# Performance work log

Measured on AMD Instinct MI355X. Metric: run time of the kernel, lower is better.

## Reference

```python
import jax, jax.numpy as jnp
import numpy as np

D_IN, D_KQ, D_V = 1024, 1024, 1024
SEQ = 4096


def setup_inputs() -> dict:
    key = jax.random.key(0)
    k1, k2, k3, k4 = jax.random.split(key, 4)
    x = jax.random.normal(k1, (SEQ, D_IN), dtype=jnp.float32)
    # original uses torch.rand (uniform [0,1)) for params
    W_query = jax.random.uniform(k2, (D_IN, D_KQ), dtype=jnp.float32)
    W_key = jax.random.uniform(k3, (D_IN, D_KQ), dtype=jnp.float32)
    W_value = jax.random.uniform(k4, (D_IN, D_V), dtype=jnp.float32)
    return {"x": x, "W_query": W_query, "W_key": W_key, "W_value": W_value}


def reference(x, W_query, W_key, W_value):
    # x: [S, d_in]
    queries = x @ W_query          # [S, d_kq]
    keys = x @ W_key               # [S, d_kq]
    values = x @ W_value           # [S, d_v]
    scale = 1.0 / jnp.sqrt(jnp.asarray(D_KQ, dtype=x.dtype))
    attn_scores = (queries @ keys.T) * scale   # [S, S]
    attn_weights = jax.nn.softmax(attn_scores, axis=-1)
    return attn_weights @ values   # [S, d_v]
```

## Files before the change

### kernel.cpp

```cpp
#include <hip/hip_runtime.h>


typedef _Float16 f16;
typedef f16 f16x8 __attribute__((ext_vector_type(8)));
typedef f16 f16x4v __attribute__((ext_vector_type(4)));
typedef float f32x4 __attribute__((ext_vector_type(4)));
typedef float f32x16 __attribute__((ext_vector_type(16)));
typedef unsigned short u16;
typedef u16 u16x8 __attribute__((ext_vector_type(8)));

extern __shared__ char dsm[];

__device__ __forceinline__ void split_f32(float v, f16& h, f16& l) {
  h = (f16)v;
  l = (f16)(v - (float)h);
}

__device__ __forceinline__ void gload16(const void* g, void* l) {
  __builtin_amdgcn_global_load_lds(
      (const __attribute__((address_space(1))) void*)g,
      (__attribute__((address_space(3))) void*)l, 16, 0, 0);
}

__global__ __launch_bounds__(256) void k_prep(
    const float* __restrict__ x, const float* __restrict__ Wq,
    const float* __restrict__ Wk, const float* __restrict__ Wv,
    f16* __restrict__ xh, f16* __restrict__ xl, f16* __restrict__ wqh,
    f16* __restrict__ wql, f16* __restrict__ wkh, f16* __restrict__ wkl,
    f16* __restrict__ wvt, float* __restrict__ sa, float* __restrict__ sb) {
  const int y = blockIdx.y;
  if (y <= 2) {
    const float* __restrict__ src = (y == 0) ? x : (y == 1) ? Wq : Wk;
    f16* __restrict__ oh = (y == 0) ? xh : (y == 1) ? wqh : wkh;
    f16* __restrict__ ol = (y == 0) ? xl : (y == 1) ? wql : wkl;
    const int n4 = (y == 0) ? (4096 * 1024 / 4) : (1024 * 1024 / 4);
    for (int i = blockIdx.x * 256 + threadIdx.x; i < n4; i += 1024 * 256) {
      float4 f = ((const float4*)src)[i];
      f16x4v h, l;
      f16 hh, ll;
      split_f32(f.x, hh, ll); h[0] = hh; l[0] = ll;
      split_f32(f.y, hh, ll); h[1] = hh; l[1] = ll;
      split_f32(f.z, hh, ll); h[2] = hh; l[2] = ll;
      split_f32(f.w, hh, ll); h[3] = hh; l[3] = ll;
      ((f16x4v*)oh)[i] = h;
      ((f16x4v*)ol)[i] = l;
    }
  } else if (y == 3) {
    if (blockIdx.x >= 256) return;
    __shared__ float sh[64][65];
    const int kb = (blockIdx.x >> 4) * 64, nb = (blockIdx.x & 15) * 64;
    const int t = threadIdx.x;
    const int r = t >> 2, c4 = (t & 3) * 16;
#pragma unroll
    for (int i = 0; i < 4; ++i) {
      float4 f = *(const float4*)&Wv[(size_t)(kb + r) * 1024 + nb + c4 + i * 4];
      sh[r][c4 + i * 4 + 0] = f.x;
      sh[r][c4 + i * 4 + 1] = f.y;
      sh[r][c4 + i * 4 + 2] = f.z;
      sh[r][c4 + i * 4 + 3] = f.w;
    }
    __syncthreads();
    const int n = t >> 2, ks = (t & 3) * 16;
    u16x8 h0, h1;
#pragma unroll
    for (int i = 0; i < 8; ++i) {
      h0[i] = __builtin_bit_cast(u16, (f16)sh[ks + i][n]);
      h1[i] = __builtin_bit_cast(u16, (f16)sh[ks + 8 + i][n]);
    }
    const size_t o = (size_t)(nb + n) * 1024 + kb + ks;
    *(u16x8*)&wvt[o] = h0;
    *(u16x8*)&wvt[o + 8] = h1;
  } else {
    if (blockIdx.x >= 512) return;
    const int z = blockIdx.x >> 8;
    const float* __restrict__ W = z ? Wk : Wq;
    float* __restrict__ o = z ? sb : sa;
    const int row = (blockIdx.x & 255) * 4 + (threadIdx.x >> 6);
    const int lane = threadIdx.x & 63;
    const float4* src = (const float4*)(W + (size_t)row * 1024);
    float s = 0.f;
#pragma unroll
    for (int i = 0; i < 4; ++i) {
      float4 f = src[lane + 64 * i];
      s += f.x + f.y + f.z + f.w;
    }
#pragma unroll
    for (int off = 1; off < 64; off <<= 1) s += __shfl_xor(s, off, 64);
    if (lane == 0) o[row] = s - 512.0f;
  }
}

__global__ __launch_bounds__(256) void k_rpq(
    const float* __restrict__ x, const float* __restrict__ sa,
    const float* __restrict__ sb, float* __restrict__ rv,
    float* __restrict__ pv, float* __restrict__ qv) {
  const int row = blockIdx.x * 4 + (threadIdx.x >> 6);
  const int lane = threadIdx.x & 63;
  const float* xr = x + (size_t)row * 1024;
  float sr = 0.f, sp = 0.f, sq = 0.f;
#pragma unroll
  for (int i = 0; i < 4; ++i) {
    const int c = (lane + 64 * i) * 4;
    float4 f = *(const float4*)&xr[c];
    float4 a = *(const float4*)&sa[c];
    float4 b = *(const float4*)&sb[c];
    sr += f.x + f.y + f.z + f.w;
    sp += f.x * a.x + f.y * a.y + f.z * a.z + f.w * a.w;
    sq += f.x * b.x + f.y * b.y + f.z * b.z + f.w * b.w;
  }
#pragma unroll
  for (int off = 1; off < 64; off <<= 1) {
    sr += __shfl_xor(sr, off, 64);
    sp += __shfl_xor(sp, off, 64);
    sq += __shfl_xor(sq, off, 64);
  }
  if (lane == 0) {
    rv[row] = sr;
    pv[row] = sp;
    qv[row] = sq;
  }
}

__global__ __launch_bounds__(512, 1) void k_qkt(
    const f16* __restrict__ Ah, const f16* __restrict__ Bx,
    const float* __restrict__ rv, const float* __restrict__ pv,
    const float* __restrict__ qv, f16* __restrict__ Pt,
    float* __restrict__ mtile, float* __restrict__ tsum) {
  char* smem = dsm;
  constexpr int K = 1024, N = 4096, nT = 32, BUF = 32768;
  const int tid = threadIdx.x;
  const int lane = tid & 63, wv = tid >> 6;
  const int bid = blockIdx.x;
  const int wg = (bid & 7) * 32 + (bid >> 3);
  const int bx = wg >> 4, by = wg & 15;
  const int brow = bx * 256, bcol = by * 256;

  const int srow16 = lane >> 2;
  const int sslot = (lane & 3) ^ ((lane >> 3) & 3);

  const f16* bases[2] = {Ah, Bx};
  const int rbase[2] = {brow, bcol};

  auto stage2 = [&](int buf, int t, int half) {
    const int kt = t * 32;
    char* bb = smem + BUF * buf;
#pragma unroll
    for (int j = 0; j < 2; ++j) {
      const int g = wv * 4 + half * 2 + j;
      const int rg = g >> 4, gm = g & 15;
      gload16(
          bases[rg] + (size_t)(rbase[rg] + gm * 16 + srow16) * K + kt + 8 * sslot,
          bb + rg * 16384 + gm * 1024);
    }
  };

  f32x16 acc[8] = {};
  const int l31 = lane & 31, ch0 = lane >> 5;
  const int arow = wv * 32 + l31;

  stage2(0, 0, 0);
  stage2(0, 0, 1);

  for (int t = 0; t < nT; ++t) {
    const int cur = t & 1;
    const char* bb = smem + BUF * cur;
    const bool pre = t < nT - 1;
    if (pre) {
      stage2(cur ^ 1, t + 1, 0);
      __builtin_amdgcn_sched_barrier(0);
      asm volatile("s_waitcnt vmcnt(2)" ::: "memory");
    } else {
      asm volatile("s_waitcnt vmcnt(0)" ::: "memory");
    }
    __builtin_amdgcn_sched_barrier(0);
    __builtin_amdgcn_s_barrier();
    __builtin_amdgcn_sched_barrier(0);

    f16x8 a_h0, b_h0[8];
    {
      const int ch = ch0;
      a_h0 = *(const f16x8*)(bb + arow * 64 + 16 * (ch ^ ((arow >> 1) & 3)));
#pragma unroll
      for (int fn = 0; fn < 8; ++fn) {
        const int r = fn * 32 + l31;
        b_h0[fn] = *(const f16x8*)(bb + 16384 + r * 64 +
                                   16 * (ch ^ ((r >> 1) & 3)));
      }
    }
    if (pre) stage2(cur ^ 1, t + 1, 1);
    asm volatile("s_waitcnt lgkmcnt(0)" ::: "memory");
    __builtin_amdgcn_sched_barrier(0);
    __builtin_amdgcn_s_setprio(1);
#pragma unroll
    for (int fn = 0; fn < 8; ++fn)
      acc[fn] = __builtin_amdgcn_mfma_f32_32x32x16_f16(a_h0, b_h0[fn], acc[fn],
                                                       0, 0, 0);
    __builtin_amdgcn_s_setprio(0);

    f16x8 a_h1, b_h1[8];
    {
      const int ch = 2 + ch0;
      a_h1 = *(const f16x8*)(bb + arow * 64 + 16 * (ch ^ ((arow >> 1) & 3)));
#pragma unroll
      for (int fn = 0; fn < 8; ++fn) {
        const int r = fn * 32 + l31;
        b_h1[fn] = *(const f16x8*)(bb + 16384 + r * 64 +
                                   16 * (ch ^ ((r >> 1) & 3)));
      }
    }
    asm volatile("s_waitcnt lgkmcnt(0)" ::: "memory");
    __builtin_amdgcn_sched_barrier(0);
    __builtin_amdgcn_s_setprio(1);
#pragma unroll
    for (int fn = 0; fn < 8; ++fn)
      acc[fn] = __builtin_amdgcn_mfma_f32_32x32x16_f16(a_h1, b_h1[fn], acc[fn],
                                                       0, 0, 0);
    __builtin_amdgcn_s_setprio(0);
    __builtin_amdgcn_sched_barrier(0);
    __builtin_amdgcn_s_barrier();
  }

  float rc[8], qc[8];
#pragma unroll
  for (int fn = 0; fn < 8; ++fn) {
    const int col = bcol + fn * 32 + l31;
    rc[fn] = rv[col];
    qc[fn] = qv[col];
  }
  const int rowbase = brow + wv * 32;
#pragma unroll
  for (int j = 0; j < 16; ++j) {
    const int rl = (j & 3) + 8 * (j >> 2) + 4 * ch0;
    const int row = rowbase + rl;
    const float rr = rv[row], pr = pv[row];
    float s[8];
    float m = -3.4e38f;
#pragma unroll
    for (int fn = 0; fn < 8; ++fn) {
      s[fn] = acc[fn][j] + 8.0f * rr * rc[fn] + (pr * rc[fn] + rr * qc[fn]) * 0.015625f;
      m = fmaxf(m, s[fn]);
    }
#pragma unroll
    for (int off = 1; off < 32; off <<= 1) m = fmaxf(m, __shfl_xor(m, off, 64));
    float sm = 0.f;
#pragma unroll
    for (int fn = 0; fn < 8; ++fn) {
      const float e = __expf(s[fn] - m);
      sm += e;
      Pt[(size_t)row * N + bcol + fn * 32 + l31] = (f16)e;
    }
#pragma unroll
    for (int off = 1; off < 32; off <<= 1) sm += __shfl_xor(sm, off, 64);
    if (l31 == 0) {
      mtile[row * 16 + by] = m;
      tsum[row * 16 + by] = sm;
    }
  }
}

__global__ __launch_bounds__(512, 1) void k_pvs(const f16* __restrict__ P,
                                                const f16* __restrict__ Vt,
                                                const float* __restrict__ mtile,
                                                const float* __restrict__ tsum,
                                                float* __restrict__ out) {
  char* smem = dsm;
  constexpr int K = 4096, nT = K / 32, BUF = 16384;
  const int tid = threadIdx.x;
  const int lane = tid & 63, wv = tid >> 6;
  const int wm = wv >> 2, wn = wv & 3;
  const int bid = blockIdx.x;
  const int wg = (bid & 7) * 32 + (bid >> 3);
  const int bx = wg >> 3, by = wg & 7;
  const int brow = bx * 128, bcol = by * 128;

  const int srow16 = lane >> 2;
  const int sslot = (lane & 3) ^ ((lane >> 3) & 3);
  const int sreg = wv >> 2;
  const f16* __restrict__ sbase = sreg ? Vt : P;
  const int rbase = sreg ? bcol : brow;

  float* sc_lds = (float*)(smem + 4 * BUF);
  if (tid < 128) {
    const int row = brow + tid;
    float mt[16], ts[16];
    float m = -3.4e38f;
#pragma unroll
    for (int t4 = 0; t4 < 4; ++t4) {
      float4 v = *(const float4*)&mtile[row * 16 + t4 * 4];
      float4 w = *(const float4*)&tsum[row * 16 + t4 * 4];
      mt[t4 * 4 + 0] = v.x; mt[t4 * 4 + 1] = v.y;
      mt[t4 * 4 + 2] = v.z; mt[t4 * 4 + 3] = v.w;
      ts[t4 * 4 + 0] = w.x; ts[t4 * 4 + 1] = w.y;
      ts[t4 * 4 + 2] = w.z; ts[t4 * 4 + 3] = w.w;
      m = fmaxf(m, fmaxf(fmaxf(v.x, v.y), fmaxf(v.z, v.w)));
    }
    float sum = 0.f;
#pragma unroll
    for (int t = 0; t < 16; ++t) sum += ts[t] * __expf(mt[t] - m);
    const float inv = 1.0f / sum;
#pragma unroll
    for (int t = 0; t < 16; ++t)
      sc_lds[t * 128 + tid] = __expf(mt[t] - m) * inv;
  }
  __syncthreads();

  auto stage = [&](int buf, int t) {
    const int kt = t * 32;
    char* bb = smem + BUF * buf + sreg * 8192;
#pragma unroll
    for (int j = 0; j < 2; ++j) {
      const int g = (wv & 3) * 2 + j;
      gload16(sbase + (size_t)(rbase + g * 16 + srow16) * K + kt + 8 * sslot,
              bb + g * 1024);
    }
  };

  f32x16 accp[2] = {};
  f32x16 accf[2] = {};
  const int l31 = lane & 31, ch0 = lane >> 5;
  const int arow0 = wm * 64 + l31;
  const int brow0 = wn * 32 + l31;

  stage(0, 0);
  stage(1, 1);
  stage(2, 2);

  for (int t = 0; t < nT; ++t) {
    const int rem = nT - 1 - t;
    if (rem >= 3) stage((t + 3) & 3, t + 3);
    __builtin_amdgcn_sched_barrier(0);
    if (rem >= 3) {
      asm volatile("s_waitcnt vmcnt(6)" ::: "memory");
    } else if (rem == 2) {
      asm volatile("s_waitcnt vmcnt(4)" ::: "memory");
    } else if (rem == 1) {
      asm volatile("s_waitcnt vmcnt(2)" ::: "memory");
    } else {
      asm volatile("s_waitcnt vmcnt(0)" ::: "memory");
    }
    __builtin_amdgcn_sched_barrier(0);
    __builtin_amdgcn_s_barrier();
    __builtin_amdgcn_sched_barrier(0);
    const char* bb = smem + BUF * (t & 3);
#pragma unroll
    for (int ks = 0; ks < 2; ++ks) {
      const int ch = ks * 2 + ch0;
      f16x8 a_h[2], b_h;
#pragma unroll
      for (int fm = 0; fm < 2; ++fm) {
        const int r = arow0 + fm * 32;
        a_h[fm] = *(const f16x8*)(bb + r * 64 + 16 * (ch ^ ((r >> 1) & 3)));
      }
      b_h = *(const f16x8*)(bb + 8192 + brow0 * 64 +
                            16 * (ch ^ ((brow0 >> 1) & 3)));
      __builtin_amdgcn_sched_barrier(0);
      asm volatile("s_waitcnt lgkmcnt(0)" ::: "memory");
      __builtin_amdgcn_sched_barrier(0);
      __builtin_amdgcn_s_setprio(1);
#pragma unroll
      for (int fm = 0; fm < 2; ++fm)
        accp[fm] = __builtin_amdgcn_mfma_f32_32x32x16_f16(a_h[fm], b_h,
                                                          accp[fm], 0, 0, 0);
      __builtin_amdgcn_s_setprio(0);
      __builtin_amdgcn_sched_barrier(0);
    }
    if ((t & 7) == 7) {
      const int tc = t >> 3;
#pragma unroll
      for (int fm = 0; fm < 2; ++fm)
#pragma unroll
        for (int j = 0; j < 16; ++j) {
          const int rloc =
              wm * 64 + fm * 32 + (j & 3) + 8 * (j >> 2) + 4 * ch0;
          accf[fm][j] += sc_lds[tc * 128 + rloc] * accp[fm][j];
          accp[fm][j] = 0.0f;
        }
    }
    __builtin_amdgcn_s_barrier();
  }

#pragma unroll
  for (int fm = 0; fm < 2; ++fm) {
    const int col = bcol + wn * 32 + l31;
#pragma unroll
    for (int j = 0; j < 16; ++j) {
      const int row =
          brow + wm * 64 + fm * 32 + (j & 3) + 8 * (j >> 2) + 4 * ch0;
      out[(size_t)row * 1024 + col] = accf[fm][j];
    }
  }
}

template <int K, int NBY>
__global__ __launch_bounds__(512, 1) void pipe_bt(const f16* __restrict__ A,
                                                  const f16* __restrict__ B,
                                                  f16* __restrict__ outh,
                                                  int ldo) {
  char* smem = dsm;
  constexpr int nT = K / 32, BUF = 16384;
  const int tid = threadIdx.x;
  const int lane = tid & 63, wv = tid >> 6;
  const int wm = wv >> 2, wn = wv & 3;
  const int bid = blockIdx.x;
  const int wg = (bid & 7) * 32 + (bid >> 3);
  const int bx = wg / NBY, by = wg % NBY;
  const int brow = bx * 128, bcol = by * 128;

  const int srow16 = lane >> 2;
  const int sslot = (lane & 3) ^ ((lane >> 3) & 3);
  const int sreg = wv >> 2;
  const f16* __restrict__ sbase = sreg ? B : A;
  const int rbase = sreg ? bcol : brow;

  auto stage = [&](int buf, int t) {
    const int kt = t * 32;
    char* bb = smem + BUF * buf + sreg * 8192;
#pragma unroll
    for (int j = 0; j < 2; ++j) {
      const int g = (wv & 3) * 2 + j;
      gload16(sbase + (size_t)(rbase + g * 16 + srow16) * K + kt + 8 * sslot,
              bb + g * 1024);
    }
  };

  f32x16 acc[2] = {};
  const int l31 = lane & 31, ch0 = lane >> 5;
  const int arow0 = wm * 64 + l31;
  const int brow0 = wn * 32 + l31;

  stage(0, 0);
  stage(1, 1);
  stage(2, 2);

  for (int t = 0; t < nT; ++t) {
    const int rem = nT - 1 - t;
    if (rem >= 3) stage((t + 3) & 3, t + 3);
    __builtin_amdgcn_sched_barrier(0);
    if (rem >= 3) {
      asm volatile("s_waitcnt vmcnt(6)" ::: "memory");
    } else if (rem == 2) {
      asm volatile("s_waitcnt vmcnt(4)" ::: "memory");
    } else if (rem == 1) {
      asm volatile("s_waitcnt vmcnt(2)" ::: "memory");
    } else {
      asm volatile("s_waitcnt vmcnt(0)" ::: "memory");
    }
    __builtin_amdgcn_sched_barrier(0);
    __builtin_amdgcn_s_barrier();
    __builtin_amdgcn_sched_barrier(0);
    const char* bb = smem + BUF * (t & 3);
#pragma unroll
    for (int ks = 0; ks < 2; ++ks) {
      const int ch = ks * 2 + ch0;
      f16x8 a_h[2], b_h;
#pragma unroll
      for (int fm = 0; fm < 2; ++fm) {
        const int r = arow0 + fm * 32;
        a_h[fm] = *(const f16x8*)(bb + r * 64 + 16 * (ch ^ ((r >> 1) & 3)));
      }
      b_h = *(const f16x8*)(bb + 8192 + brow0 * 64 +
                            16 * (ch ^ ((brow0 >> 1) & 3)));
      __builtin_amdgcn_sched_barrier(0);
      asm volatile("s_waitcnt lgkmcnt(0)" ::: "memory");
      __builtin_amdgcn_sched_barrier(0);
      __builtin_amdgcn_s_setprio(1);
#pragma unroll
      for (int fm = 0; fm < 2; ++fm)
        acc[fm] = __builtin_amdgcn_mfma_f32_32x32x16_f16(a_h[fm], b_h, acc[fm],
                                                         0, 0, 0);
      __builtin_amdgcn_s_setprio(0);
      __builtin_amdgcn_sched_barrier(0);
    }
    __builtin_amdgcn_s_barrier();
  }

#pragma unroll
  for (int fm = 0; fm < 2; ++fm) {
    const int col = bcol + wn * 32 + l31;
#pragma unroll
    for (int j = 0; j < 16; ++j) {
      const int row =
          brow + wm * 64 + fm * 32 + (j & 3) + 8 * (j >> 2) + 4 * ch0;
      outh[(size_t)row * ldo + col] = (f16)acc[fm][j];
    }
  }
}

template <int NM, int OUT>
__global__ __launch_bounds__(256) void gemm_bt(
    const f16* __restrict__ A, const f16* __restrict__ Al,
    const f16* __restrict__ B, const f16* __restrict__ Bl, int K,
    f16* __restrict__ oh, f16* __restrict__ ol, int ldo, float scale,
    const float* __restrict__ sav, const float* __restrict__ sbv) {
  f16* smem = (f16*)dsm;
  f16* tAh = smem;
  f16* tBh = smem + 8192;
  f16* tAl = smem + 16384;
  f16* tBl = smem + 24576;

  const int tid = threadIdx.x;
  const int lane = tid & 63, wid = tid >> 6;
  const int wr = wid >> 1, wc = wid & 1;
  const int brow = blockIdx.x * 128, bcol = blockIdx.y * 128;
  const int ar = lane & 15, k0 = (lane >> 4) * 8;
  const int crow = lane >> 3, ccol = (lane & 7) * 8;

  f32x4 acc[4][4] = {};
  const size_t aoff = (size_t)crow * K + ccol;

  for (int kt = 0; kt < K; kt += 64) {
    const f16* Ab = A + (size_t)brow * K + kt;
    const f16* Bb = B + (size_t)bcol * K + kt;
#pragma unroll
    for (int cc = 0; cc < 4; ++cc) {
      const int c = wid * 4 + cc;
      const size_t co = (size_t)c * 8 * K + aoff;
      gload16(Ab + co, tAh + c * 512);
      gload16(Bb + co, tBh + c * 512);
      if constexpr (NM >= 2) gload16(Al + (size_t)brow * K + kt + co, tAl + c * 512);
      if constexpr (NM == 3) gload16(Bl + (size_t)bcol * K + kt + co, tBl + c * 512);
    }
    __syncthreads();
#pragma unroll
    for (int ks = 0; ks < 2; ++ks) {
      f16x8 ah[4], bh[4], alv[4], blv[4];
#pragma unroll
      for (int m = 0; m < 4; ++m) {
        ah[m] = *(const f16x8*)&tAh[(wr * 64 + m * 16 + ar) * 64 + ks * 32 + k0];
        bh[m] = *(const f16x8*)&tBh[(wc * 64 + m * 16 + ar) * 64 + ks * 32 + k0];
        if constexpr (NM >= 2)
          alv[m] = *(const f16x8*)&tAl[(wr * 64 + m * 16 + ar) * 64 + ks * 32 + k0];
        if constexpr (NM == 3)
          blv[m] = *(const f16x8*)&tBl[(wc * 64 + m * 16 + ar) * 64 + ks * 32 + k0];
      }
#pragma unroll
      for (int m = 0; m < 4; ++m)
#pragma unroll
        for (int n = 0; n < 4; ++n) {
          acc[m][n] = __builtin_amdgcn_mfma_f32_16x16x32_f16(ah[m], bh[n], acc[m][n], 0, 0, 0);
          if constexpr (NM >= 2)
            acc[m][n] = __builtin_amdgcn_mfma_f32_16x16x32_f16(alv[m], bh[n], acc[m][n], 0, 0, 0);
          if constexpr (NM == 3)
            acc[m][n] = __builtin_amdgcn_mfma_f32_16x16x32_f16(ah[m], blv[n], acc[m][n], 0, 0, 0);
        }
    }
    __syncthreads();
  }

#pragma unroll
  for (int m = 0; m < 4; ++m)
#pragma unroll
    for (int n = 0; n < 4; ++n)
#pragma unroll
      for (int j = 0; j < 4; ++j) {
        const int row = brow + wr * 64 + m * 16 + (lane >> 4) * 4 + j;
        const int col = bcol + wc * 64 + n * 16 + ar;
        const size_t idx = (size_t)row * ldo + col;
        if constexpr (OUT == 1) {
          f16 h, l;
          split_f32(acc[m][n][j] * scale, h, l);
          oh[idx] = h;
          ol[idx] = l;
        } else if constexpr (OUT == 2) {
          oh[idx] = (f16)(acc[m][n][j] * scale);
        } else {
          const float v =
              (acc[m][n][j] - 256.0f - 0.5f * sav[col] - 0.5f * sbv[row]) * scale;
          oh[idx] = (f16)v;
        }
      }
}

extern "C" void kernel_launch(void* const* d_in, const int* in_sizes, int n_in,
                              void* d_out, int out_size, void* d_ws,
                              size_t ws_size, hipStream_t stream) {
  const float* x = (const float*)d_in[0];
  const float* Wq = (const float*)d_in[1];
  const float* Wk = (const float*)d_in[2];
  const float* Wv = (const float*)d_in[3];
  float* out = (float*)d_out;
  char* ws = (char*)d_ws;
  const size_t MiB = 1u << 20;
  f16* xh = (f16*)(ws + 0 * MiB);
  f16* xl = (f16*)(ws + 8 * MiB);
  f16* Th = (f16*)(ws + 16 * MiB);
  f16* Vt = (f16*)(ws + 32 * MiB);
  f16* Pt = (f16*)(ws + 40 * MiB);
  float* mtile = (float*)(ws + 72 * MiB);
  float* tsum = (float*)(ws + 73 * MiB);
  f16* Wqh = (f16*)(ws + 40 * MiB);
  f16* Wql = (f16*)(ws + 42 * MiB);
  f16* Wkh = (f16*)(ws + 44 * MiB);
  f16* Wkl = (f16*)(ws + 46 * MiB);
  f16* Mth = (f16*)(ws + 48 * MiB);
  f16* Wtvh = (f16*)(ws + 52 * MiB);
  float* sa = (float*)(ws + 54 * MiB);
  float* sb = (float*)(ws + 54 * MiB + 65536);
  float* rv = (float*)(ws + 8 * MiB);
  float* pv = (float*)(ws + 8 * MiB + 65536);
  float* qv = (float*)(ws + 8 * MiB + 131072);

  (void)hipFuncSetAttribute((const void*)k_qkt,
                            hipFuncAttributeMaxDynamicSharedMemorySize, 65536);
  (void)hipFuncSetAttribute((const void*)k_pvs,
                            hipFuncAttributeMaxDynamicSharedMemorySize, 73728);
  (void)hipFuncSetAttribute((const void*)pipe_bt<1024, 32>,
                            hipFuncAttributeMaxDynamicSharedMemorySize, 65536);

  k_prep<<<dim3(1024, 5), 256, 0, stream>>>(x, Wq, Wk, Wv, xh, xl, Wqh, Wql,
                                            Wkh, Wkl, Wtvh, sa, sb);
  gemm_bt<3, 4><<<dim3(8, 8), 256, 65536, stream>>>(
      Wkh, Wkl, Wqh, Wql, 1024, Mth, nullptr, 1024, 0.03125f, sa, sb);
  gemm_bt<2, 2><<<dim3(32, 8), 256, 49152, stream>>>(
      xh, xl, Mth, nullptr, 1024, Th, nullptr, 1024, 1.0f, nullptr, nullptr);
  pipe_bt<1024, 32><<<dim3(256), 512, 65536, stream>>>(Wtvh, xh, Vt, 4096);
  k_rpq<<<dim3(1024), 256, 0, stream>>>(x, sa, sb, rv, pv, qv);
  k_qkt<<<dim3(256), 512, 65536, stream>>>(Th, xh, rv, pv, qv, Pt, mtile,
                                           tsum);
  k_pvs<<<dim3(256), 512, 73728, stream>>>(Pt, Vt, mtile, tsum, out);
}
```

Baseline: 214.6 us.

## Split K across two wave groups in PV GEMM with larger 64x64 warp tiles

Reworks the P·V kernel so each wave computes a 64x64 output sub-tile (2x2 MFMA fragments) instead of 64x32, and the two halves of the workgroup each take alternate K-slices of 64. The partial sums are reduced through LDS at the end. Stages are now 64 wide, with a 32KB buffer per stage. This raises MFMA work per LDS fragment load and halves the barrier count per K step. In exchange it needs about 136KB of LDS and more accumulator registers, and adds a final LDS reduction.

```diff
diff --git a/kernel.cpp b/kernel.cpp
--- a/kernel.cpp
+++ b/kernel.cpp
@@ -258,26 +258,21 @@
   }
 }
 
-__global__ __launch_bounds__(512, 1) void k_pvs(const f16* __restrict__ P,
+__global__ __launch_bounds__(512, 2) void k_pvs(const f16* __restrict__ P,
                                                 const f16* __restrict__ Vt,
                                                 const float* __restrict__ mtile,
                                                 const float* __restrict__ tsum,
                                                 float* __restrict__ out) {
   char* smem = dsm;
-  constexpr int K = 4096, nT = K / 32, BUF = 16384;
+  constexpr int K = 4096, BUF = 32768, NP = 32;
   const int tid = threadIdx.x;
   const int lane = tid & 63, wv = tid >> 6;
-  const int wm = wv >> 2, wn = wv & 3;
+  const int qd = wv >> 2, wq = wv & 3;
+  const int wr = wq >> 1, wc = wq & 1;
   const int bid = blockIdx.x;
   const int wg = (bid & 7) * 32 + (bid >> 3);
   const int bx = wg >> 3, by = wg & 7;
   const int brow = bx * 128, bcol = by * 128;
-
-  const int srow16 = lane >> 2;
-  const int sslot = (lane & 3) ^ ((lane >> 3) & 3);
-  const int sreg = wv >> 2;
-  const f16* __restrict__ sbase = sreg ? Vt : P;
-  const int rbase = sreg ? bcol : brow;
 
   float* sc_lds = (float*)(smem + 4 * BUF);
   if (tid < 128) {
@@ -304,90 +299,118 @@
   }
   __syncthreads();
 
-  auto stage = [&](int buf, int t) {
-    const int kt = t * 32;
-    char* bb = smem + BUF * buf + sreg * 8192;
-#pragma unroll
-    for (int j = 0; j < 2; ++j) {
-      const int g = (wv & 3) * 2 + j;
-      gload16(sbase + (size_t)(rbase + g * 16 + srow16) * K + kt + 8 * sslot,
-              bb + g * 1024);
+  const int srow8 = lane >> 3;
+  const int scol8 = lane & 7;
+
+  auto stage = [&](int t) {
+    const int kt = t * 64;
+    char* bb = smem + BUF * (t & 3);
+#pragma unroll
+    for (int j = 0; j < 4; ++j) {
+      const int g = wv * 4 + j;
+      const int rg = g >> 4, gm = g & 15;
+      const int r = gm * 8 + srow8;
+      const f16* base = rg ? Vt : P;
+      const int rowb = rg ? bcol : brow;
+      const int sc = scol8 ^ ((r >> 1) & 7);
+      gload16(base + (size_t)(rowb + r) * K + kt + 8 * sc,
+              bb + rg * 16384 + gm * 1024);
     }
   };
 
-  f32x16 accp[2] = {};
-  f32x16 accf[2] = {};
+  f32x16 accp[2][2] = {};
+  f32x16 accf[2][2] = {};
   const int l31 = lane & 31, ch0 = lane >> 5;
-  const int arow0 = wm * 64 + l31;
-  const int brow0 = wn * 32 + l31;
-
-  stage(0, 0);
-  stage(1, 1);
-  stage(2, 2);
-
-  for (int t = 0; t < nT; ++t) {
-    const int rem = nT - 1 - t;
-    if (rem >= 3) stage((t + 3) & 3, t + 3);
-    __builtin_amdgcn_sched_barrier(0);
-    if (rem >= 3) {
-      asm volatile("s_waitcnt vmcnt(6)" ::: "memory");
-    } else if (rem == 2) {
+  const int ar0 = wr * 64 + l31;
+  const int br0 = wc * 64 + l31;
+
+  stage(0);
+  stage(1);
+
+  for (int p = 0; p < NP; ++p) {
+    const bool pre = p < NP - 1;
+    if (pre) {
+      stage(2 * p + 2);
+      __builtin_amdgcn_sched_barrier(0);
       asm volatile("s_waitcnt vmcnt(4)" ::: "memory");
-    } else if (rem == 1) {
-      asm volatile("s_waitcnt vmcnt(2)" ::: "memory");
     } else {
       asm volatile("s_waitcnt vmcnt(0)" ::: "memory");
     }
     __builtin_amdgcn_sched_barrier(0);
     __builtin_amdgcn_s_barrier();
     __builtin_amdgcn_sched_barrier(0);
-    const char* bb = smem + BUF * (t & 3);
-#pragma unroll
-    for (int ks = 0; ks < 2; ++ks) {
+    const char* bb = smem + BUF * ((2 * p + qd) & 3);
+#pragma unroll
+    for (int ks = 0; ks < 4; ++ks) {
       const int ch = ks * 2 + ch0;
-      f16x8 a_h[2], b_h;
+      f16x8 a[2], b[2];
 #pragma unroll
       for (int fm = 0; fm < 2; ++fm) {
-        const int r = arow0 + fm * 32;
-        a_h[fm] = *(const f16x8*)(bb + r * 64 + 16 * (ch ^ ((r >> 1) & 3)));
+        const int r = ar0 + fm * 32;
+        a[fm] = *(const f16x8*)(bb + r * 128 + 16 * (ch ^ ((r >> 1) & 7)));
       }
-      b_h = *(const f16x8*)(bb + 8192 + brow0 * 64 +
-                            16 * (ch ^ ((brow0 >> 1) & 3)));
-      __builtin_amdgcn_sched_barrier(0);
+#pragma unroll
+      for (int fn = 0; fn < 2; ++fn) {
+        const int r = br0 + fn * 32;
+        b[fn] = *(const f16x8*)(bb + 16384 + r * 128 +
+                                16 * (ch ^ ((r >> 1) & 7)));
+      }
+      if (ks == 0 && pre) stage(2 * p + 3);
       asm volatile("s_waitcnt lgkmcnt(0)" ::: "memory");
       __builtin_amdgcn_sched_barrier(0);
       __builtin_amdgcn_s_setprio(1);
 #pragma unroll
       for (int fm = 0; fm < 2; ++fm)
-        accp[fm] = __builtin_amdgcn_mfma_f32_32x32x16_f16(a_h[fm], b_h,
-                                                          accp[fm], 0, 0, 0);
+#pragma unroll
+        for (int fn = 0; fn < 2; ++fn)
+          accp[fm][fn] = __builtin_amdgcn_mfma_f32_32x32x16_f16(
+              a[fm], b[fn], accp[fm][fn], 0, 0, 0);
       __builtin_amdgcn_s_setprio(0);
-      __builtin_amdgcn_sched_barrier(0);
-    }
-    if ((t & 7) == 7) {
-      const int tc = t >> 3;
+    }
+    if (p & 1) {
+      const int tc = p >> 1;
 #pragma unroll
       for (int fm = 0; fm < 2; ++fm)
 #pragma unroll
+        for (int fn = 0; fn < 2; ++fn)
+#pragma unroll
+          for (int j = 0; j < 16; ++j) {
+            const int rloc =
+                wr * 64 + fm * 32 + (j & 3) + 8 * (j >> 2) + 4 * ch0;
+            accf[fm][fn][j] += sc_lds[tc * 128 + rloc] * accp[fm][fn][j];
+            accp[fm][fn][j] = 0.0f;
+          }
+    }
+    __builtin_amdgcn_sched_barrier(0);
+    __builtin_amdgcn_s_barrier();
+  }
+
+  float* red = (float*)smem;
+  if (qd == 1) {
+#pragma unroll
+    for (int fm = 0; fm < 2; ++fm)
+#pragma unroll
+      for (int fn = 0; fn < 2; ++fn)
+#pragma unroll
+        for (int j = 0; j < 16; ++j)
+          red[wq * 4096 + (fm * 2 + fn) * 1024 + j * 64 + lane] =
+              accf[fm][fn][j];
+  }
+  __syncthreads();
+  if (qd == 0) {
+#pragma unroll
+    for (int fm = 0; fm < 2; ++fm)
+#pragma unroll
+      for (int fn = 0; fn < 2; ++fn)
+#pragma unroll
         for (int j = 0; j < 16; ++j) {
-          const int rloc =
-              wm * 64 + fm * 32 + (j & 3) + 8 * (j >> 2) + 4 * ch0;
-          accf[fm][j] += sc_lds[tc * 128 + rloc] * accp[fm][j];
-          accp[fm][j] = 0.0f;
+          const float v = accf[fm][fn][j] +
+                          red[wq * 4096 + (fm * 2 + fn) * 1024 + j * 64 + lane];
+          const int row =
+              brow + wr * 64 + fm * 32 + (j & 3) + 8 * (j >> 2) + 4 * ch0;
+          const int col = bcol + wc * 64 + fn * 32 + l31;
+          out[(size_t)row * 1024 + col] = v;
         }
-    }
-    __builtin_amdgcn_s_barrier();
-  }
-
-#pragma unroll
-  for (int fm = 0; fm < 2; ++fm) {
-    const int col = bcol + wn * 32 + l31;
-#pragma unroll
-    for (int j = 0; j < 16; ++j) {
-      const int row =
-          brow + wm * 64 + fm * 32 + (j & 3) + 8 * (j >> 2) + 4 * ch0;
-      out[(size_t)row * 1024 + col] = accf[fm][j];
-    }
   }
 }
 
@@ -603,7 +626,7 @@
   (void)hipFuncSetAttribute((const void*)k_qkt,
                             hipFuncAttributeMaxDynamicSharedMemorySize, 65536);
   (void)hipFuncSetAttribute((const void*)k_pvs,
-                            hipFuncAttributeMaxDynamicSharedMemorySize, 73728);
+                            hipFuncAttributeMaxDynamicSharedMemorySize, 139264);
   (void)hipFuncSetAttribute((const void*)pipe_bt<1024, 32>,
                             hipFuncAttributeMaxDynamicSharedMemorySize, 65536);
 
@@ -617,5 +640,5 @@
   k_rpq<<<dim3(1024), 256, 0, stream>>>(x, sa, sb, rv, pv, qv);
   k_qkt<<<dim3(256), 512, 65536, stream>>>(Th, xh, rv, pv, qv, Pt, mtile,
                                            tsum);
-  k_pvs<<<dim3(256), 512, 73728, stream>>>(Pt, Vt, mtile, tsum, out);
-}
+  k_pvs<<<dim3(256), 512, 139264, stream>>>(Pt, Vt, mtile, tsum, out);
+}
```

Result: faster. 199.9 us (-6.8%).
